# Kernel optimization log

Hardware: AMD Instinct MI355X
Metric: run time of the kernel (lower is better)

The kernel has to match this reference:

```python
import jax, jax.numpy as jnp
import numpy as np

N, E, F, H, O = 50000, 800000, 64, 128, 64
GRID_SIZE, SPLINE_ORDER = 3, 2


def make_grid(in_features, grid_size=GRID_SIZE, spline_order=SPLINE_ORDER, grid_range=(-1.0, 1.0)):
    h = (grid_range[1] - grid_range[0]) / grid_size
    pts = jnp.arange(-spline_order, grid_size + spline_order + 1, dtype=jnp.float32) * h + grid_range[0]
    return jnp.tile(pts[None, :], (in_features, 1))  # [in, grid_size + 2*order + 1]


def b_splines(x, grid, spline_order=SPLINE_ORDER):
    # x: [B, in], grid: [in, G+2k+1] -> bases [B, in, G+k]
    xe = x[..., None]
    bases = ((xe >= grid[:, :-1]) & (xe < grid[:, 1:])).astype(x.dtype)
    for k in range(1, spline_order + 1):
        bases = ((xe - grid[:, : -(k + 1)]) / (grid[:, k:-1] - grid[:, : -(k + 1)]) * bases[..., :-1]
                 + (grid[:, k + 1:] - xe) / (grid[:, k + 1:] - grid[:, 1:-k]) * bases[..., 1:])
    return bases


def setup_inputs() -> dict:
    key = jax.random.key(0)
    ks = jax.random.split(key, 12)
    x = jax.random.normal(ks[0], (N, F), dtype=jnp.float32)
    contexts = jax.random.normal(ks[1], (E, F), dtype=jnp.float32)
    attn = jax.random.uniform(ks[2], (E,), dtype=jnp.float32)
    seg_ids = jnp.sort(jax.random.randint(ks[3], (E,), 0, N, dtype=jnp.int32))
    s = 0.05
    Wn = jax.random.normal(ks[4], (H, F), dtype=jnp.float32) * s
    bn = jnp.zeros((H,), dtype=jnp.float32)
    Wc = jax.random.normal(ks[5], (H, F), dtype=jnp.float32) * s
    bc = jnp.zeros((H,), dtype=jnp.float32)
    Wu = jax.random.normal(ks[6], (O, H), dtype=jnp.float32) * s
    bu = jnp.zeros((O,), dtype=jnp.float32)
    n_coef = GRID_SIZE + SPLINE_ORDER
    base_w = jax.random.normal(ks[7], (O, O), dtype=jnp.float32) * s
    spline_w = jax.random.normal(ks[8], (O, O, n_coef), dtype=jnp.float32) * s
    spline_scaler = jnp.ones((O, O), dtype=jnp.float32)
    grid = make_grid(O)
    return dict(x=x, contexts=contexts, attn=attn, seg_ids=seg_ids, Wn=Wn, bn=bn,
                Wc=Wc, bc=bc, Wu=Wu, bu=bu, base_w=base_w, spline_w=spline_w,
                spline_scaler=spline_scaler, grid=grid)


def reference(x, contexts, attn, seg_ids, Wn, bn, Wc, bc, Wu, bu, base_w, spline_w, spline_scaler, grid):
    n = x.shape[0]
    # per-edge context transform, attention weighting
    ctx_t = contexts @ Wc.T + bc                      # [E, H]
    weighted = ctx_t * attn[:, None]                  # [E, H]
    seg_sum = jax.ops.segment_sum(weighted, seg_ids, num_segments=n)        # [N, H]
    deg = jax.ops.segment_sum(jnp.ones_like(attn), seg_ids, num_segments=n)  # [N]
    ctx_agg = seg_sum / jnp.maximum(deg, 1.0)[:, None]  # mean over edges per node
    x_t = x @ Wn.T + bn                               # [N, H]
    upd = (x_t + ctx_agg) @ Wu.T + bu                 # [N, O]
    # KANLinear (efficient-kan): silu base path + b-spline path
    base_out = jax.nn.silu(upd) @ base_w.T            # [N, O]
    bases = b_splines(upd, grid)                      # [N, O, G+k]
    scaled_sw = spline_w * spline_scaler[..., None]   # [O, O, G+k]
    spline_out = jnp.einsum('bik,oik->bo', bases, scaled_sw)
    kan_out = base_out + spline_out
    # nodes with no contexts keep their raw features (num_features == output_dim)
    return jnp.where(deg[:, None] > 0, kan_out, x)
```

## Files before the change

### kernel.cpp

```cpp
#include <hip/hip_runtime.h>
#include <hip/hip_bf16.h>

#define NN 50000
#define NE 800000

typedef short short8 __attribute__((ext_vector_type(8)));
typedef float f32x4 __attribute__((ext_vector_type(4)));
typedef unsigned short ushort_t;

static __device__ __forceinline__ unsigned bits(float f) { return __float_as_uint(f); }
static __device__ __forceinline__ float hi_f(float v) {
  return __uint_as_float(bits(v) & 0xFFFF0000u);
}
static __device__ __forceinline__ ushort_t hi_u(float v) { return (ushort_t)(bits(v) >> 16); }
static __device__ __forceinline__ unsigned pack_hi(float v0, float v1) {
  return (bits(v0) >> 16) | (bits(v1) & 0xFFFF0000u);
}
static __device__ __forceinline__ unsigned pack_lo(float v0, float v1) {
  float l0 = v0 - hi_f(v0), l1 = v1 - hi_f(v1);
  return (bits(l0) >> 16) | (bits(l1) & 0xFFFF0000u);
}

#define MFMA(a, b, c) __builtin_amdgcn_mfma_f32_16x16x32_bf16(a, b, c, 0, 0, 0)

__global__ __launch_bounds__(256) void kA_pack_off(
    const float* __restrict__ Wn, const float* __restrict__ Wc,
    const float* __restrict__ Wu, const float* __restrict__ base_w,
    const float* __restrict__ spline_w, const float* __restrict__ scaler,
    const int* __restrict__ seg,
    ushort_t* __restrict__ p1h, ushort_t* __restrict__ p2h,
    ushort_t* __restrict__ p3h, int* __restrict__ off) {
  int t = blockIdx.x * 256 + threadIdx.x;
  if (t < 4096) {
    int l = t & 63, lm = l & 15, lk = l >> 4;
    if (t < 2048) {
      int nt = t >> 8, ks = (t >> 6) & 3;
      int h = nt * 16 + lm;
#pragma unroll
      for (int j = 0; j < 8; ++j) {
        int f = ks * 32 + lk * 8 + j;
        float v = (f < 64) ? Wn[h * 64 + f] : Wc[h * 64 + (f - 64)];
        p1h[t * 8 + j] = hi_u(v);
      }
    }
    if (t < 1024) {
      int nt = t >> 8, ks = (t >> 6) & 3;
      int o = nt * 16 + lm;
#pragma unroll
      for (int j = 0; j < 8; ++j) {
        int hh = ks * 32 + lk * 8 + j;
        p2h[t * 8 + j] = hi_u(Wu[o * 128 + hh]);
      }
    }
    if (t < 3072) {
      int nt = t / 768, ks = (t >> 6) % 12;
      int o = nt * 16 + lm;
#pragma unroll
      for (int j = 0; j < 8; ++j) {
        int k = ks * 32 + lk * 8 + j;
        int i = k / 6, c = k % 6;
        float v = (c == 0) ? base_w[o * 64 + i]
                           : spline_w[(o * 64 + i) * 5 + (c - 1)] * scaler[o * 64 + i];
        p3h[t * 8 + j] = hi_u(v);
      }
    }
  }
  int e = t;
  if (e < NE) {
    int s1 = seg[e];
    if (e == 0) {
      for (int n = 0; n <= s1; ++n) off[n] = 0;
    } else {
      int s0 = seg[e - 1];
      for (int n = s0 + 1; n <= s1; ++n) off[n] = e;
    }
    if (e == NE - 1) {
      for (int n = s1 + 1; n <= NN; ++n) off[n] = NE;
    }
  }
}

__global__ __launch_bounds__(256) void k1_edge_agg(
    const float* __restrict__ contexts, const float* __restrict__ attn,
    const int* __restrict__ off, ushort_t* __restrict__ Sph,
    float* __restrict__ aprime, float* __restrict__ degw) {
  int n = blockIdx.x * 4 + (threadIdx.x >> 6);
  int lane = threadIdx.x & 63;
  if (n >= NN) return;
  int s = off[n];
  int e_end = off[n + 1];
  int deg_i = e_end - s;

  int sub = lane >> 4;
  int fq = lane & 15;
  const float4* ctx4 = (const float4*)contexts;

  float4 S = make_float4(0.f, 0.f, 0.f, 0.f);
  float A = 0.f;
  if (deg_i > 0) {
    int last = e_end - 1;
    for (int e0 = s; e0 < e_end; e0 += 16) {
      float a[4];
      float4 c[4];
#pragma unroll
      for (int u = 0; u < 4; ++u) {
        int eu = e0 + 4 * u + sub;
        a[u] = (eu < e_end) ? attn[eu] : 0.f;
        c[u] = ctx4[(size_t)min(eu, last) * 16 + fq];
      }
#pragma unroll
      for (int u = 0; u < 4; ++u) {
        S.x += a[u] * c[u].x;
        S.y += a[u] * c[u].y;
        S.z += a[u] * c[u].z;
        S.w += a[u] * c[u].w;
        A += a[u];
      }
    }
  }
#pragma unroll
  for (int m = 16; m <= 32; m <<= 1) {
    S.x += __shfl_xor(S.x, m);
    S.y += __shfl_xor(S.y, m);
    S.z += __shfl_xor(S.z, m);
    S.w += __shfl_xor(S.w, m);
    A += __shfl_xor(A, m);
  }
  float deg = (float)deg_i;
  float inv = 1.f / fmaxf(deg, 1.f);
  if (lane < 16) {
    float ox = S.x * inv, oy = S.y * inv, oz = S.z * inv, ow = S.w * inv;
    uint2 hp;
    hp.x = pack_hi(ox, oy);
    hp.y = pack_hi(oz, ow);
    *(uint2*)&Sph[(size_t)n * 64 + lane * 4] = hp;
  }
  if (lane == 0) { aprime[n] = A * inv; degw[n] = deg; }
}

__global__ __launch_bounds__(256, 4) void k234(
    const float* __restrict__ x,
    const ushort_t* __restrict__ Sph,
    const float* __restrict__ aprime, const float* __restrict__ degw,
    const float* __restrict__ bn, const float* __restrict__ bc,
    const float* __restrict__ bu,
    const ushort_t* __restrict__ p1h, const ushort_t* __restrict__ p2h,
    const ushort_t* __restrict__ p3h,
    const float* __restrict__ gridp, float* __restrict__ out) {
  __shared__ __align__(16) unsigned char arena[32768];
  __shared__ float ap[64], degl[64];
  ushort_t* Uh = (ushort_t*)arena;
  ushort_t* Ul = (ushort_t*)(arena + 16384);
  ushort_t* Vh = (ushort_t*)arena;
  float*    ot = (float*)(arena + 24576);

  int tid = threadIdx.x;
  int n0 = blockIdx.x * 64;
  int w = tid >> 6, l = tid & 63;
  int lm = l & 15, lk = l >> 4;
  const short8* P1h = (const short8*)p1h;
  const short8* P2h = (const short8*)p2h;
  const short8* P3h = (const short8*)p3h;

  short8 B2[4];
#pragma unroll
  for (int ks = 0; ks < 4; ++ks) B2[ks] = P2h[(w * 4 + ks) * 64 + l];

  {
    const float4* x4 = (const float4*)x;
    const uint4* Sh4 = (const uint4*)Sph;
    for (int q = tid; q < 1024; q += 256) {
      int row = q >> 4, slot = q & 15;
      int n = n0 + row;
      int idx = (row * 128 + slot * 8) ^ ((row & 7) << 3);
      if (slot < 8) {
        float4 a = make_float4(0.f, 0.f, 0.f, 0.f), b = a;
        if (n < NN) {
          a = x4[(size_t)n * 16 + slot * 2];
          b = x4[(size_t)n * 16 + slot * 2 + 1];
        }
        uint4 hp, lp;
        hp.x = pack_hi(a.x, a.y); hp.y = pack_hi(a.z, a.w);
        hp.z = pack_hi(b.x, b.y); hp.w = pack_hi(b.z, b.w);
        lp.x = pack_lo(a.x, a.y); lp.y = pack_lo(a.z, a.w);
        lp.z = pack_lo(b.x, b.y); lp.w = pack_lo(b.z, b.w);
        *(uint4*)&Uh[idx] = hp;
        *(uint4*)&Ul[idx] = lp;
      } else {
        uint4 vh = make_uint4(0u, 0u, 0u, 0u);
        if (n < NN) vh = Sh4[(size_t)n * 8 + (slot & 7)];
        *(uint4*)&Uh[idx] = vh;
      }
    }
  }
  if (tid < 64) {
    int n = n0 + tid;
    ap[tid] = (n < NN) ? aprime[n] : 0.f;
    degl[tid] = (n < NN) ? degw[n] : 1.f;
  }
  __syncthreads();

  int swzA = (lm & 7) << 3;

  f32x4 acc1[2][4];
#pragma unroll
  for (int q = 0; q < 2; ++q)
#pragma unroll
    for (int mt = 0; mt < 4; ++mt) acc1[q][mt] = (f32x4){0.f, 0.f, 0.f, 0.f};
#pragma unroll
  for (int ks = 0; ks < 4; ++ks) {
    short8 bh0 = P1h[((2 * w + 0) * 4 + ks) * 64 + l];
    short8 bh1 = P1h[((2 * w + 1) * 4 + ks) * 64 + l];
#pragma unroll
    for (int mt = 0; mt < 4; ++mt) {
      int ai = ((mt * 16 + lm) * 128 + ks * 32 + lk * 8) ^ swzA;
      short8 ah = *(const short8*)&Uh[ai];
      acc1[0][mt] = MFMA(ah, bh0, acc1[0][mt]);
      acc1[1][mt] = MFMA(ah, bh1, acc1[1][mt]);
      if (ks < 2) {
        short8 al = *(const short8*)&Ul[ai];
        acc1[0][mt] = MFMA(al, bh0, acc1[0][mt]);
        acc1[1][mt] = MFMA(al, bh1, acc1[1][mt]);
      }
    }
  }
  __syncthreads();

#pragma unroll
  for (int q = 0; q < 2; ++q) {
    int h = (2 * w + q) * 16 + lm;
    float bnv = bn[h], bcv = bc[h];
#pragma unroll
    for (int mt = 0; mt < 4; ++mt) {
#pragma unroll
      for (int r = 0; r < 4; ++r) {
        int node = mt * 16 + lk * 4 + r;
        float t = acc1[q][mt][r] + bnv + ap[node] * bcv;
        Ul[(node * 128 + h) ^ ((node & 7) << 3)] = hi_u(t);
      }
    }
  }
  __syncthreads();

  f32x4 acc2[4];
#pragma unroll
  for (int mt = 0; mt < 4; ++mt) acc2[mt] = (f32x4){0.f, 0.f, 0.f, 0.f};
#pragma unroll
  for (int ks = 0; ks < 4; ++ks) {
#pragma unroll
    for (int mt = 0; mt < 4; ++mt) {
      int ai = ((mt * 16 + lm) * 128 + ks * 32 + lk * 8) ^ swzA;
      short8 ah = *(const short8*)&Ul[ai];
      acc2[mt] = MFMA(ah, B2[ks], acc2[mt]);
    }
  }
  __syncthreads();

  float g[8];
#pragma unroll
  for (int j = 0; j < 8; ++j) g[j] = gridp[j];
  float r1[7], r2[6];
#pragma unroll
  for (int j = 0; j < 7; ++j) r1[j] = 1.f / (g[j + 1] - g[j]);
#pragma unroll
  for (int j = 0; j < 6; ++j) r2[j] = 1.f / (g[j + 2] - g[j]);
  float buv = bu[w * 16 + lm];

#pragma unroll
  for (int half = 0; half < 2; ++half) {
#pragma unroll
    for (int ms = 0; ms < 2; ++ms) {
      int mt = half * 2 + ms;
#pragma unroll
      for (int r = 0; r < 4; ++r) {
        float xv = acc2[mt][r] + buv;
        float sil = xv / (1.f + __expf(-xv));
        float b0[7], b1[6], b2[5];
#pragma unroll
        for (int q = 0; q < 7; ++q) b0[q] = (xv >= g[q] && xv < g[q + 1]) ? 1.f : 0.f;
#pragma unroll
        for (int q = 0; q < 6; ++q)
          b1[q] = (xv - g[q]) * r1[q] * b0[q] + (g[q + 2] - xv) * r1[q + 1] * b0[q + 1];
#pragma unroll
        for (int q = 0; q < 5; ++q)
          b2[q] = (xv - g[q]) * r2[q] * b1[q] + (g[q + 3] - xv) * r2[q + 1] * b1[q + 1];
        int ln = ms * 16 + lk * 4 + r;
        int base = ln * 384 + (w * 16 + lm) * 6;
        int sw = (ln & 7) << 3;
        *(unsigned*)&Vh[(base + 0) ^ sw] = pack_hi(sil, b2[0]);
        *(unsigned*)&Vh[(base + 2) ^ sw] = pack_hi(b2[1], b2[2]);
        *(unsigned*)&Vh[(base + 4) ^ sw] = pack_hi(b2[3], b2[4]);
      }
    }
    __syncthreads();

    f32x4 accK[2];
    accK[0] = (f32x4){0.f, 0.f, 0.f, 0.f};
    accK[1] = (f32x4){0.f, 0.f, 0.f, 0.f};
#pragma unroll
    for (int ks = 0; ks < 12; ++ks) {
      short8 bh = P3h[(w * 12 + ks) * 64 + l];
#pragma unroll
      for (int s = 0; s < 2; ++s) {
        int ri = ((s * 16 + lm) * 384 + ks * 32 + lk * 8) ^ swzA;
        short8 ah = *(const short8*)&Vh[ri];
        accK[s] = MFMA(ah, bh, accK[s]);
      }
    }
    __syncthreads();

#pragma unroll
    for (int s = 0; s < 2; ++s) {
      int o = w * 16 + lm;
#pragma unroll
      for (int r = 0; r < 4; ++r) {
        int ln = s * 16 + lk * 4 + r;
        ot[(ln * 64 + o) ^ ((ln & 7) << 3)] = accK[s][r];
      }
    }
    __syncthreads();

    {
      int row2 = tid >> 3, c8 = (tid & 7) * 8;
      int node = half * 32 + row2;
      int n = n0 + node;
      if (n < NN) {
        int sw = (row2 & 7) << 3;
        float4 v0 = *(float4*)&ot[((row2 * 64 + c8) ^ sw)];
        float4 v1 = *(float4*)&ot[((row2 * 64 + c8 + 4) ^ sw)];
        if (degl[node] <= 0.f) {
          v0 = *(const float4*)(x + (size_t)n * 64 + c8);
          v1 = *(const float4*)(x + (size_t)n * 64 + c8 + 4);
        }
        *(float4*)(out + (size_t)n * 64 + c8) = v0;
        *(float4*)(out + (size_t)n * 64 + c8 + 4) = v1;
      }
    }
    __syncthreads();
  }
}

extern "C" void kernel_launch(void* const* d_in, const int* in_sizes, int n_in,
                              void* d_out, int out_size, void* d_ws, size_t ws_size,
                              hipStream_t stream) {
  const float* x        = (const float*)d_in[0];
  const float* contexts = (const float*)d_in[1];
  const float* attn     = (const float*)d_in[2];
  const int*   seg      = (const int*)d_in[3];
  const float* Wn       = (const float*)d_in[4];
  const float* bn       = (const float*)d_in[5];
  const float* Wc       = (const float*)d_in[6];
  const float* bc       = (const float*)d_in[7];
  const float* Wu       = (const float*)d_in[8];
  const float* bu       = (const float*)d_in[9];
  const float* base_w   = (const float*)d_in[10];
  const float* spline_w = (const float*)d_in[11];
  const float* scaler   = (const float*)d_in[12];
  const float* gridp    = (const float*)d_in[13];
  float* out = (float*)d_out;

  ushort_t* us  = (ushort_t*)d_ws;
  ushort_t* Sph = us;
  ushort_t* p1h = Sph + 3200000;
  ushort_t* p2h = p1h + 16384;
  ushort_t* p3h = p2h + 8192;
  float* aprime = (float*)(p3h + 24576);
  float* degw   = aprime + 50000;
  int*   off    = (int*)(degw + 50000);

  kA_pack_off<<<3125, 256, 0, stream>>>(Wn, Wc, Wu, base_w, spline_w, scaler, seg,
                                        p1h, p2h, p3h, off);
  k1_edge_agg<<<12500, 256, 0, stream>>>(contexts, attn, off, Sph, aprime, degw);
  k234<<<782, 256, 0, stream>>>(x, Sph, aprime, degw, bn, bc, bu,
                                p1h, p2h, p3h, gridp, out);
}
```

Baseline: 66.54 us.

## Halve node tile per block in fused dense kernel to raise occupancy

The fused node kernel now handles 32 nodes per block instead of 64, doubling the grid and removing the two-half loop. Shared memory shrinks to 24 KB, the first-layer output goes to a separate LDS region so one barrier can be dropped, and launch bounds are raised to 6 blocks per CU. Per-block weight fragment loads are repeated across twice as many blocks, which adds global/L2 traffic in exchange for more parallelism and better latency hiding.

```diff
diff --git a/kernel.cpp b/kernel.cpp
--- a/kernel.cpp
+++ b/kernel.cpp
@@ -138,7 +138,7 @@
   if (lane == 0) { aprime[n] = A * inv; degw[n] = deg; }
 }
 
-__global__ __launch_bounds__(256, 4) void k234(
+__global__ __launch_bounds__(256, 6) void k234(
     const float* __restrict__ x,
     const ushort_t* __restrict__ Sph,
     const float* __restrict__ aprime, const float* __restrict__ degw,
@@ -147,29 +147,28 @@
     const ushort_t* __restrict__ p1h, const ushort_t* __restrict__ p2h,
     const ushort_t* __restrict__ p3h,
     const float* __restrict__ gridp, float* __restrict__ out) {
-  __shared__ __align__(16) unsigned char arena[32768];
-  __shared__ float ap[64], degl[64];
+  __shared__ __align__(16) unsigned char arena[24576];
+  __shared__ float ap[32], degl[32];
   ushort_t* Uh = (ushort_t*)arena;
-  ushort_t* Ul = (ushort_t*)(arena + 16384);
+  ushort_t* Ul = (ushort_t*)(arena + 8192);
+  ushort_t* Th = (ushort_t*)(arena + 16384);
   ushort_t* Vh = (ushort_t*)arena;
-  float*    ot = (float*)(arena + 24576);
+  float*    ot = (float*)arena;
 
   int tid = threadIdx.x;
-  int n0 = blockIdx.x * 64;
+  int n0 = blockIdx.x * 32;
   int w = tid >> 6, l = tid & 63;
   int lm = l & 15, lk = l >> 4;
   const short8* P1h = (const short8*)p1h;
   const short8* P2h = (const short8*)p2h;
   const short8* P3h = (const short8*)p3h;
-
-  short8 B2[4];
-#pragma unroll
-  for (int ks = 0; ks < 4; ++ks) B2[ks] = P2h[(w * 4 + ks) * 64 + l];
+  int swzA = (lm & 7) << 3;
 
   {
     const float4* x4 = (const float4*)x;
     const uint4* Sh4 = (const uint4*)Sph;
-    for (int q = tid; q < 1024; q += 256) {
+#pragma unroll
+    for (int q = tid; q < 512; q += 256) {
       int row = q >> 4, slot = q & 15;
       int n = n0 + row;
       int idx = (row * 128 + slot * 8) ^ ((row & 7) << 3);
@@ -193,26 +192,24 @@
       }
     }
   }
-  if (tid < 64) {
+  if (tid < 32) {
     int n = n0 + tid;
     ap[tid] = (n < NN) ? aprime[n] : 0.f;
     degl[tid] = (n < NN) ? degw[n] : 1.f;
   }
   __syncthreads();
 
-  int swzA = (lm & 7) << 3;
-
-  f32x4 acc1[2][4];
+  f32x4 acc1[2][2];
 #pragma unroll
   for (int q = 0; q < 2; ++q)
 #pragma unroll
-    for (int mt = 0; mt < 4; ++mt) acc1[q][mt] = (f32x4){0.f, 0.f, 0.f, 0.f};
+    for (int mt = 0; mt < 2; ++mt) acc1[q][mt] = (f32x4){0.f, 0.f, 0.f, 0.f};
 #pragma unroll
   for (int ks = 0; ks < 4; ++ks) {
     short8 bh0 = P1h[((2 * w + 0) * 4 + ks) * 64 + l];
     short8 bh1 = P1h[((2 * w + 1) * 4 + ks) * 64 + l];
 #pragma unroll
-    for (int mt = 0; mt < 4; ++mt) {
+    for (int mt = 0; mt < 2; ++mt) {
       int ai = ((mt * 16 + lm) * 128 + ks * 32 + lk * 8) ^ swzA;
       short8 ah = *(const short8*)&Uh[ai];
       acc1[0][mt] = MFMA(ah, bh0, acc1[0][mt]);
@@ -224,34 +221,33 @@
       }
     }
   }
-  __syncthreads();
-
 #pragma unroll
   for (int q = 0; q < 2; ++q) {
     int h = (2 * w + q) * 16 + lm;
     float bnv = bn[h], bcv = bc[h];
 #pragma unroll
-    for (int mt = 0; mt < 4; ++mt) {
+    for (int mt = 0; mt < 2; ++mt) {
 #pragma unroll
       for (int r = 0; r < 4; ++r) {
         int node = mt * 16 + lk * 4 + r;
         float t = acc1[q][mt][r] + bnv + ap[node] * bcv;
-        Ul[(node * 128 + h) ^ ((node & 7) << 3)] = hi_u(t);
-      }
-    }
-  }
-  __syncthreads();
-
-  f32x4 acc2[4];
-#pragma unroll
-  for (int mt = 0; mt < 4; ++mt) acc2[mt] = (f32x4){0.f, 0.f, 0.f, 0.f};
+        Th[(node * 128 + h) ^ ((node & 7) << 3)] = hi_u(t);
+      }
+    }
+  }
+  __syncthreads();
+
+  f32x4 acc2[2];
+  acc2[0] = (f32x4){0.f, 0.f, 0.f, 0.f};
+  acc2[1] = (f32x4){0.f, 0.f, 0.f, 0.f};
 #pragma unroll
   for (int ks = 0; ks < 4; ++ks) {
-#pragma unroll
-    for (int mt = 0; mt < 4; ++mt) {
+    short8 bh = P2h[(w * 4 + ks) * 64 + l];
+#pragma unroll
+    for (int mt = 0; mt < 2; ++mt) {
       int ai = ((mt * 16 + lm) * 128 + ks * 32 + lk * 8) ^ swzA;
-      short8 ah = *(const short8*)&Ul[ai];
-      acc2[mt] = MFMA(ah, B2[ks], acc2[mt]);
+      short8 ah = *(const short8*)&Th[ai];
+      acc2[mt] = MFMA(ah, bh, acc2[mt]);
     }
   }
   __syncthreads();
@@ -267,76 +263,70 @@
   float buv = bu[w * 16 + lm];
 
 #pragma unroll
-  for (int half = 0; half < 2; ++half) {
-#pragma unroll
-    for (int ms = 0; ms < 2; ++ms) {
-      int mt = half * 2 + ms;
-#pragma unroll
-      for (int r = 0; r < 4; ++r) {
-        float xv = acc2[mt][r] + buv;
-        float sil = xv / (1.f + __expf(-xv));
-        float b0[7], b1[6], b2[5];
-#pragma unroll
-        for (int q = 0; q < 7; ++q) b0[q] = (xv >= g[q] && xv < g[q + 1]) ? 1.f : 0.f;
-#pragma unroll
-        for (int q = 0; q < 6; ++q)
-          b1[q] = (xv - g[q]) * r1[q] * b0[q] + (g[q + 2] - xv) * r1[q + 1] * b0[q + 1];
-#pragma unroll
-        for (int q = 0; q < 5; ++q)
-          b2[q] = (xv - g[q]) * r2[q] * b1[q] + (g[q + 3] - xv) * r2[q + 1] * b1[q + 1];
-        int ln = ms * 16 + lk * 4 + r;
-        int base = ln * 384 + (w * 16 + lm) * 6;
-        int sw = (ln & 7) << 3;
-        *(unsigned*)&Vh[(base + 0) ^ sw] = pack_hi(sil, b2[0]);
-        *(unsigned*)&Vh[(base + 2) ^ sw] = pack_hi(b2[1], b2[2]);
-        *(unsigned*)&Vh[(base + 4) ^ sw] = pack_hi(b2[3], b2[4]);
-      }
-    }
-    __syncthreads();
-
-    f32x4 accK[2];
-    accK[0] = (f32x4){0.f, 0.f, 0.f, 0.f};
-    accK[1] = (f32x4){0.f, 0.f, 0.f, 0.f};
-#pragma unroll
-    for (int ks = 0; ks < 12; ++ks) {
-      short8 bh = P3h[(w * 12 + ks) * 64 + l];
-#pragma unroll
-      for (int s = 0; s < 2; ++s) {
-        int ri = ((s * 16 + lm) * 384 + ks * 32 + lk * 8) ^ swzA;
-        short8 ah = *(const short8*)&Vh[ri];
-        accK[s] = MFMA(ah, bh, accK[s]);
-      }
-    }
-    __syncthreads();
-
+  for (int mt = 0; mt < 2; ++mt) {
+#pragma unroll
+    for (int r = 0; r < 4; ++r) {
+      float xv = acc2[mt][r] + buv;
+      float sil = xv / (1.f + __expf(-xv));
+      float b0[7], b1[6], b2[5];
+#pragma unroll
+      for (int q = 0; q < 7; ++q) b0[q] = (xv >= g[q] && xv < g[q + 1]) ? 1.f : 0.f;
+#pragma unroll
+      for (int q = 0; q < 6; ++q)
+        b1[q] = (xv - g[q]) * r1[q] * b0[q] + (g[q + 2] - xv) * r1[q + 1] * b0[q + 1];
+#pragma unroll
+      for (int q = 0; q < 5; ++q)
+        b2[q] = (xv - g[q]) * r2[q] * b1[q] + (g[q + 3] - xv) * r2[q + 1] * b1[q + 1];
+      int ln = mt * 16 + lk * 4 + r;
+      int base = ln * 384 + (w * 16 + lm) * 6;
+      int sw = (ln & 7) << 3;
+      *(unsigned*)&Vh[(base + 0) ^ sw] = pack_hi(sil, b2[0]);
+      *(unsigned*)&Vh[(base + 2) ^ sw] = pack_hi(b2[1], b2[2]);
+      *(unsigned*)&Vh[(base + 4) ^ sw] = pack_hi(b2[3], b2[4]);
+    }
+  }
+  __syncthreads();
+
+  f32x4 accK[2];
+  accK[0] = (f32x4){0.f, 0.f, 0.f, 0.f};
+  accK[1] = (f32x4){0.f, 0.f, 0.f, 0.f};
+#pragma unroll
+  for (int ks = 0; ks < 12; ++ks) {
+    short8 bh = P3h[(w * 12 + ks) * 64 + l];
 #pragma unroll
     for (int s = 0; s < 2; ++s) {
-      int o = w * 16 + lm;
-#pragma unroll
-      for (int r = 0; r < 4; ++r) {
-        int ln = s * 16 + lk * 4 + r;
-        ot[(ln * 64 + o) ^ ((ln & 7) << 3)] = accK[s][r];
-      }
-    }
-    __syncthreads();
-
-    {
-      int row2 = tid >> 3, c8 = (tid & 7) * 8;
-      int node = half * 32 + row2;
-      int n = n0 + node;
-      if (n < NN) {
-        int sw = (row2 & 7) << 3;
-        float4 v0 = *(float4*)&ot[((row2 * 64 + c8) ^ sw)];
-        float4 v1 = *(float4*)&ot[((row2 * 64 + c8 + 4) ^ sw)];
-        if (degl[node] <= 0.f) {
-          v0 = *(const float4*)(x + (size_t)n * 64 + c8);
-          v1 = *(const float4*)(x + (size_t)n * 64 + c8 + 4);
-        }
-        *(float4*)(out + (size_t)n * 64 + c8) = v0;
-        *(float4*)(out + (size_t)n * 64 + c8 + 4) = v1;
-      }
-    }
-    __syncthreads();
+      int ri = ((s * 16 + lm) * 384 + ks * 32 + lk * 8) ^ swzA;
+      short8 ah = *(const short8*)&Vh[ri];
+      accK[s] = MFMA(ah, bh, accK[s]);
+    }
+  }
+  __syncthreads();
+
+#pragma unroll
+  for (int s = 0; s < 2; ++s) {
+    int o = w * 16 + lm;
+#pragma unroll
+    for (int r = 0; r < 4; ++r) {
+      int ln = s * 16 + lk * 4 + r;
+      ot[(ln * 64 + o) ^ ((ln & 7) << 3)] = accK[s][r];
+    }
+  }
+  __syncthreads();
+
+  {
+    int row2 = tid >> 3, c8 = (tid & 7) * 8;
+    int n = n0 + row2;
+    if (n < NN) {
+      int sw = (row2 & 7) << 3;
+      float4 v0 = *(float4*)&ot[((row2 * 64 + c8) ^ sw)];
+      float4 v1 = *(float4*)&ot[((row2 * 64 + c8 + 4) ^ sw)];
+      if (degl[row2] <= 0.f) {
+        v0 = *(const float4*)(x + (size_t)n * 64 + c8);
+        v1 = *(const float4*)(x + (size_t)n * 64 + c8 + 4);
+      }
+      *(float4*)(out + (size_t)n * 64 + c8) = v0;
+      *(float4*)(out + (size_t)n * 64 + c8 + 4) = v1;
+    }
   }
 }
 
@@ -371,6 +361,6 @@
   kA_pack_off<<<3125, 256, 0, stream>>>(Wn, Wc, Wu, base_w, spline_w, scaler, seg,
                                         p1h, p2h, p3h, off);
   k1_edge_agg<<<12500, 256, 0, stream>>>(contexts, attn, off, Sph, aprime, degw);
-  k234<<<782, 256, 0, stream>>>(x, Sph, aprime, degw, bn, bc, bu,
-                                p1h, p2h, p3h, gridp, out);
-}
+  k234<<<1563, 256, 0, stream>>>(x, Sph, aprime, degw, bn, bc, bu,
+                                 p1h, p2h, p3h, gridp, out);
+}
```

New measurement: 67.54 us. Within noise of the previous version (+1.5%).
